# Kernel optimization log

Hardware: AMD Instinct MI355X
Metric: run time of the kernel (lower is better)

Reference implementation:

```python
import jax, jax.numpy as jnp
import numpy as np

B, S, D = 4, 2048, 1024
H, DK, DV = 16, 64, 64
EPS = 1e-6


def setup_inputs() -> dict:
    key = jax.random.key(0)
    ks = jax.random.split(key, 7)
    sc = 0.02
    return {
        "q": jax.random.normal(ks[0], (B, S, D), jnp.float32),
        "k": jax.random.normal(ks[1], (B, S, D), jnp.float32),
        "v": jax.random.normal(ks[2], (B, S, D), jnp.float32),
        "Wq": jax.random.normal(ks[3], (D, H * DK), jnp.float32) * sc,
        "Wk": jax.random.normal(ks[4], (D, H * DK), jnp.float32) * sc,
        "Wv": jax.random.normal(ks[5], (D, H * DV), jnp.float32) * sc,
        "Wo": jax.random.normal(ks[6], (H * DV, D), jnp.float32) * sc,
        "ln_gamma": jnp.ones((D,), jnp.float32),
        "ln_beta": jnp.zeros((D,), jnp.float32),
    }


def reference(q, k, v, Wq, Wk, Wv, Wo, ln_gamma, ln_beta):
    residual = q
    # QKV projections -> [b, h, s, d]
    qh = (q @ Wq).reshape(B, S, H, DK).transpose(0, 2, 1, 3)
    kh = (k @ Wk).reshape(B, S, H, DK).transpose(0, 2, 1, 3)
    vh = (v @ Wv).reshape(B, S, H, DV).transpose(0, 2, 1, 3)
    temperature = jnp.sqrt(jnp.float32(DK))
    # scaled dot-product attention (reverse=False, dropout = eval identity)
    scores = jnp.einsum('bhqd,bhkd->bhqk', qh / temperature, kh)
    attn = jax.nn.softmax(scores, axis=-1)
    ctx = jnp.einsum('bhqk,bhkd->bhqd', attn, vh)
    # merge heads and output projection
    ctx = ctx.transpose(0, 2, 1, 3).reshape(B, S, H * DV)
    out = ctx @ Wo + residual
    # LayerNorm eps=1e-6
    mu = out.mean(-1, keepdims=True)
    var = out.var(-1, keepdims=True)
    out = (out - mu) / jnp.sqrt(var + EPS) * ln_gamma + ln_beta
    return out
```

## Files before the change

### kernel.cpp

```cpp
#include <hip/hip_runtime.h>

typedef __bf16 bf16x8 __attribute__((ext_vector_type(8)));
typedef __bf16 bf16x4 __attribute__((ext_vector_type(4)));
typedef float  f32x4  __attribute__((ext_vector_type(4)));

#define MFMA16(a, b, c) __builtin_amdgcn_mfma_f32_16x16x32_bf16(a, b, c, 0, 0, 0)
#define AS1(p) ((__attribute__((address_space(1))) void*)(p))
#define AS3(p) ((__attribute__((address_space(3))) void*)(p))

union U8 { uint u[4]; bf16x8 v; };
union U4 { bf16x4 h[2]; bf16x8 v; };

__device__ inline uint packbf(float a, float b) {
  union { __bf16 h[2]; uint u; } x;
  x.h[0] = (__bf16)a; x.h[1] = (__bf16)b; return x.u;
}

__global__ __launch_bounds__(256) void cvt_kernel(const float* __restrict__ in,
                                                  __bf16* __restrict__ out, int n4) {
  int i = blockIdx.x * blockDim.x + threadIdx.x;
  if (i < n4) {
    float4 v = ((const float4*)in)[i];
    bf16x4 o = {(__bf16)v.x, (__bf16)v.y, (__bf16)v.z, (__bf16)v.w};
    *(bf16x4*)(out + (size_t)i * 4) = o;
  }
}

__global__ void wtrans_kernel(const float* __restrict__ in, __bf16* __restrict__ out) {
  __shared__ __bf16 t[64][65];
  int bx = blockIdx.x * 64, by = blockIdx.y * 64;
  int tx = threadIdx.x;
  for (int ty = threadIdx.y; ty < 64; ty += 4)
    t[ty][tx] = (__bf16)in[(size_t)(by + ty) * 1024 + bx + tx];
  __syncthreads();
  for (int ty = threadIdx.y; ty < 64; ty += 4)
    out[(size_t)(bx + ty) * 1024 + by + tx] = t[tx][ty];
}

template <int MODE>
__global__ __launch_bounds__(256) void gemm128_kernel(
    const __bf16* __restrict__ A, const __bf16* __restrict__ BT,
    __bf16* __restrict__ Cb, float* __restrict__ Cf,
    const float* __restrict__ resid, int M, int N, int K) {
  __shared__ __bf16 As[128 * 32];
  __shared__ __bf16 Bs[128 * 32];
  const int t = threadIdx.x, l = t & 63, w = t >> 6;
  const int lr = l & 15, lg = l >> 4;
  const int brow = blockIdx.y * 128, bcol = blockIdx.x * 128;
  const int wr = w >> 1, wc = w & 1;
  f32x4 acc[4][4] = {};

  const int srow = w * 16 + (l >> 2);
  const int scol = (l & 3) * 8;
  const __bf16* Ag = A + (size_t)(brow + srow) * K + scol;
  const __bf16* Bg = BT + (size_t)(bcol + srow) * K + scol;
  __bf16* Asw = As + w * 512;
  __bf16* Bsw = Bs + w * 512;

  for (int k0 = 0; k0 < K; k0 += 32) {
    __builtin_amdgcn_global_load_lds(AS1(Ag + k0), AS3(Asw), 16, 0, 0);
    __builtin_amdgcn_global_load_lds(AS1(Ag + k0 + (size_t)64 * K), AS3(Asw + 2048), 16, 0, 0);
    __builtin_amdgcn_global_load_lds(AS1(Bg + k0), AS3(Bsw), 16, 0, 0);
    __builtin_amdgcn_global_load_lds(AS1(Bg + k0 + (size_t)64 * K), AS3(Bsw + 2048), 16, 0, 0);
    __syncthreads();
    bf16x8 a[4], b[4];
#pragma unroll
    for (int m = 0; m < 4; ++m)
      a[m] = *(const bf16x8*)(As + (wr * 64 + m * 16 + lr) * 32 + lg * 8);
#pragma unroll
    for (int n = 0; n < 4; ++n)
      b[n] = *(const bf16x8*)(Bs + (wc * 64 + n * 16 + lr) * 32 + lg * 8);
#pragma unroll
    for (int m = 0; m < 4; ++m)
#pragma unroll
      for (int n = 0; n < 4; ++n)
        acc[m][n] = MFMA16(a[m], b[n], acc[m][n]);
    __syncthreads();
  }

  const int r0 = brow + wr * 64 + lg * 4;
  const int c0 = bcol + wc * 64 + lr;
#pragma unroll
  for (int m = 0; m < 4; ++m)
#pragma unroll
    for (int n = 0; n < 4; ++n) {
      if (MODE == 3) {
        const int dg = c0 + n * 16;
        const int tok = r0 + m * 16;
        bf16x4 pk4;
#pragma unroll
        for (int r = 0; r < 4; ++r) pk4[r] = (__bf16)acc[m][n][r];
        size_t idx = ((size_t)((tok >> 11) * 16 + (dg >> 6)) * 64 + (dg & 63)) * 2048 + (tok & 2047);
        *(bf16x4*)(Cb + idx) = pk4;
      } else {
#pragma unroll
        for (int r = 0; r < 4; ++r) {
          size_t idx = (size_t)(r0 + m * 16 + r) * N + c0 + n * 16;
          if (MODE == 0) Cb[idx] = (__bf16)acc[m][n][r];
          if (MODE == 2) Cb[idx] = (__bf16)(acc[m][n][r] * 0.125f);
          if (MODE == 1) Cf[idx] = acc[m][n][r] + resid[idx];
        }
      }
    }
}

__global__ __launch_bounds__(256) void attn_kernel(const __bf16* __restrict__ Qh,
                                                   const __bf16* __restrict__ Kh,
                                                   const __bf16* __restrict__ VhT,
                                                   __bf16* __restrict__ Ctx) {
  __shared__ __bf16 Vbuf[2 * 4096];
  const int t = threadIdx.x, l = t & 63, w = t >> 6;
  const int lr = l & 15, lg = l >> 4;
  const int bh = blockIdx.y;
  const size_t base = (size_t)(bh >> 4) * (2048 * 1024) + (size_t)(bh & 15) * 64;
  const int q0 = blockIdx.x * 128 + w * 32;

  bf16x8 aq[2][2];
#pragma unroll
  for (int nq = 0; nq < 2; ++nq)
#pragma unroll
    for (int kc = 0; kc < 2; ++kc)
      aq[nq][kc] = *(const bf16x8*)(Qh + base + (size_t)(q0 + nq * 16 + lr) * 1024 + kc * 32 + lg * 8);

  f32x4 o[4][2] = {};
  float rm[2] = {-1e30f, -1e30f}, rl[2] = {0.f, 0.f};

  const int l8 = l & 7, lrow = l >> 3;
  const __bf16* vsrc = VhT + (size_t)bh * 131072 + (size_t)(w * 16 + lrow) * 2048 + ((l8 ^ lrow) * 8);

  const int xorm = (l8) << 4;
  int vo[2][2];
#pragma unroll
  for (int kc = 0; kc < 2; ++kc)
#pragma unroll
    for (int h = 0; h < 2; ++h)
      vo[kc][h] = lr * 128 + ((kc * 64 + h * 32 + lg * 8) ^ xorm);

  {
    __bf16* d0 = Vbuf + w * 1024;
    __builtin_amdgcn_global_load_lds(AS1(vsrc), AS3(d0), 16, 0, 0);
    __builtin_amdgcn_global_load_lds(AS1(vsrc + 16384), AS3(d0 + 512), 16, 0, 0);
  }
  __syncthreads();

  for (int tt = 0; tt < 32; ++tt) {
    const __bf16* Vb = Vbuf + (tt & 1) * 4096;
    __bf16* Vn = Vbuf + ((tt + 1) & 1) * 4096;
    const int kv0 = tt * 64;
    const int kvn = ((tt + 1) & 31) * 64;

    __builtin_amdgcn_global_load_lds(AS1(vsrc + kvn), AS3(Vn + w * 1024), 16, 0, 0);
    __builtin_amdgcn_global_load_lds(AS1(vsrc + kvn + 16384), AS3(Vn + w * 1024 + 512), 16, 0, 0);

    bf16x8 kf[4][2];
#pragma unroll
    for (int mkv = 0; mkv < 4; ++mkv)
#pragma unroll
      for (int kc = 0; kc < 2; ++kc)
        kf[mkv][kc] = *(const bf16x8*)(Kh + base + (size_t)(kv0 + mkv * 16 + lr) * 1024 + kc * 32 + lg * 8);

    f32x4 s[2][4];
    __builtin_amdgcn_s_setprio(1);
#pragma unroll
    for (int nq = 0; nq < 2; ++nq)
#pragma unroll
      for (int mkv = 0; mkv < 4; ++mkv) {
        f32x4 acc = {};
        acc = MFMA16(kf[mkv][0], aq[nq][0], acc);
        acc = MFMA16(kf[mkv][1], aq[nq][1], acc);
        s[nq][mkv] = acc;
      }
    __builtin_amdgcn_s_setprio(0);

    uint pk[2][4][2];
#pragma unroll
    for (int nq = 0; nq < 2; ++nq) {
      float mx = s[nq][0][0];
#pragma unroll
      for (int mkv = 0; mkv < 4; ++mkv)
#pragma unroll
        for (int r = 0; r < 4; ++r) mx = fmaxf(mx, s[nq][mkv][r]);
      mx = fmaxf(mx, __shfl_xor(mx, 16));
      mx = fmaxf(mx, __shfl_xor(mx, 32));
      float nm = fmaxf(rm[nq], mx);
      float corr = __expf(rm[nq] - nm);
      rm[nq] = nm;
      float sum = 0.f;
#pragma unroll
      for (int mkv = 0; mkv < 4; ++mkv) {
        float p0 = __expf(s[nq][mkv][0] - nm);
        float p1 = __expf(s[nq][mkv][1] - nm);
        float p2 = __expf(s[nq][mkv][2] - nm);
        float p3 = __expf(s[nq][mkv][3] - nm);
        sum += (p0 + p1) + (p2 + p3);
        pk[nq][mkv][0] = packbf(p0, p1);
        pk[nq][mkv][1] = packbf(p2, p3);
      }
      sum += __shfl_xor(sum, 16);
      sum += __shfl_xor(sum, 32);
      rl[nq] = rl[nq] * corr + sum;
#pragma unroll
      for (int md = 0; md < 4; ++md) o[md][nq] *= corr;
    }

    __builtin_amdgcn_s_setprio(1);
#pragma unroll
    for (int md = 0; md < 4; ++md) {
#pragma unroll
      for (int kc = 0; kc < 2; ++kc) {
        U4 vf;
        vf.h[0] = *(const bf16x4*)((const char*)Vb + md * 2048 + vo[kc][0]);
        vf.h[1] = *(const bf16x4*)((const char*)Vb + md * 2048 + vo[kc][1]);
#pragma unroll
        for (int nq = 0; nq < 2; ++nq) {
          U8 pf;
          pf.u[0] = pk[nq][2 * kc][0];
          pf.u[1] = pk[nq][2 * kc][1];
          pf.u[2] = pk[nq][2 * kc + 1][0];
          pf.u[3] = pk[nq][2 * kc + 1][1];
          o[md][nq] = MFMA16(vf.v, pf.v, o[md][nq]);
        }
      }
    }
    __builtin_amdgcn_s_setprio(0);

    __syncthreads();
  }

  float rinv[2] = {1.f / rl[0], 1.f / rl[1]};
#pragma unroll
  for (int md = 0; md < 4; ++md)
#pragma unroll
    for (int nq = 0; nq < 2; ++nq) {
      bf16x4 pk4;
#pragma unroll
      for (int r = 0; r < 4; ++r) pk4[r] = (__bf16)(o[md][nq][r] * rinv[nq]);
      *(bf16x4*)(Ctx + base + (size_t)(q0 + nq * 16 + lr) * 1024 + md * 16 + lg * 4) = pk4;
    }
}

__global__ __launch_bounds__(256) void ln_kernel(const float* __restrict__ x,
                                                 const float* __restrict__ g,
                                                 const float* __restrict__ bta,
                                                 float* __restrict__ out) {
  __shared__ float sred[4], s2red[4];
  const int row = blockIdx.x, t = threadIdx.x;
  float4 v = ((const float4*)(x + (size_t)row * 1024))[t];
  float s = v.x + v.y + v.z + v.w;
  float s2 = v.x * v.x + v.y * v.y + v.z * v.z + v.w * v.w;
#pragma unroll
  for (int mask = 1; mask < 64; mask <<= 1) {
    s += __shfl_xor(s, mask);
    s2 += __shfl_xor(s2, mask);
  }
  if ((t & 63) == 0) { sred[t >> 6] = s; s2red[t >> 6] = s2; }
  __syncthreads();
  s = sred[0] + sred[1] + sred[2] + sred[3];
  s2 = s2red[0] + s2red[1] + s2red[2] + s2red[3];
  float mu = s * (1.f / 1024.f);
  float inv = rsqrtf(s2 * (1.f / 1024.f) - mu * mu + 1e-6f);
  float4 gv = ((const float4*)g)[t];
  float4 bv = ((const float4*)bta)[t];
  float4 ov;
  ov.x = (v.x - mu) * inv * gv.x + bv.x;
  ov.y = (v.y - mu) * inv * gv.y + bv.y;
  ov.z = (v.z - mu) * inv * gv.z + bv.z;
  ov.w = (v.w - mu) * inv * gv.w + bv.w;
  ((float4*)(out + (size_t)row * 1024))[t] = ov;
}

extern "C" void kernel_launch(void* const* d_in, const int* in_sizes, int n_in,
                              void* d_out, int out_size, void* d_ws, size_t ws_size,
                              hipStream_t stream) {
  const float* q  = (const float*)d_in[0];
  const float* k  = (const float*)d_in[1];
  const float* v  = (const float*)d_in[2];
  const float* Wq = (const float*)d_in[3];
  const float* Wk = (const float*)d_in[4];
  const float* Wv = (const float*)d_in[5];
  const float* Wo = (const float*)d_in[6];
  const float* g  = (const float*)d_in[7];
  const float* bt = (const float*)d_in[8];
  float* out = (float*)d_out;

  const int NTOK = 4 * 2048;
  const int NEL = NTOK * 1024;

  __bf16* qb  = (__bf16*)d_ws;
  __bf16* kb  = qb + NEL;
  __bf16* vb  = kb + NEL;
  __bf16* WqT = vb + NEL;
  __bf16* WkT = WqT + 1024 * 1024;
  __bf16* WvT = WkT + 1024 * 1024;
  __bf16* WoT = WvT + 1024 * 1024;
  __bf16* Qh  = WoT + 1024 * 1024;
  __bf16* Kh  = Qh + NEL;
  __bf16* VhT = Kh + NEL;
  __bf16* ctx = qb;
  float*  ao  = (float*)kb;

  cvt_kernel<<<NEL / 1024, 256, 0, stream>>>(q, qb, NEL / 4);
  cvt_kernel<<<NEL / 1024, 256, 0, stream>>>(k, kb, NEL / 4);
  cvt_kernel<<<NEL / 1024, 256, 0, stream>>>(v, vb, NEL / 4);

  dim3 wtb(64, 4), wtg(16, 16);
  wtrans_kernel<<<wtg, wtb, 0, stream>>>(Wq, WqT);
  wtrans_kernel<<<wtg, wtb, 0, stream>>>(Wk, WkT);
  wtrans_kernel<<<wtg, wtb, 0, stream>>>(Wv, WvT);
  wtrans_kernel<<<wtg, wtb, 0, stream>>>(Wo, WoT);

  dim3 gg(1024 / 128, NTOK / 128);
  gemm128_kernel<2><<<gg, 256, 0, stream>>>(qb, WqT, Qh, nullptr, nullptr, NTOK, 1024, 1024);
  gemm128_kernel<0><<<gg, 256, 0, stream>>>(kb, WkT, Kh, nullptr, nullptr, NTOK, 1024, 1024);
  gemm128_kernel<3><<<gg, 256, 0, stream>>>(vb, WvT, VhT, nullptr, nullptr, NTOK, 1024, 1024);

  attn_kernel<<<dim3(2048 / 128, 64), 256, 0, stream>>>(Qh, Kh, VhT, ctx);

  gemm128_kernel<1><<<gg, 256, 0, stream>>>(ctx, WoT, nullptr, ao, q, NTOK, 1024, 1024);

  ln_kernel<<<NTOK, 256, 0, stream>>>(ao, g, bt, out);
}
```

Measured before the change: 515.8 us.

## Drop LDS V staging, use exp2 softmax with lazy rescaling

The attention kernel no longer stages V tiles through double-buffered LDS with global_load_lds and block barriers. Each lane now reads V fragments straight from global memory into registers. The Q scale folds log2(e) into the projection epilogue so the softmax can use exp2f. Rescaling of the running max and output accumulators is skipped unless some row's max grows by more than 8, which removes per-tile correction multiplies. The trade-offs are more uncoalesced global and cache traffic for V, and larger unnormalized exponent values in bf16 P.

```diff
diff --git a/kernel.cpp b/kernel.cpp
--- a/kernel.cpp
+++ b/kernel.cpp
@@ -97,7 +97,7 @@
         for (int r = 0; r < 4; ++r) {
           size_t idx = (size_t)(r0 + m * 16 + r) * N + c0 + n * 16;
           if (MODE == 0) Cb[idx] = (__bf16)acc[m][n][r];
-          if (MODE == 2) Cb[idx] = (__bf16)(acc[m][n][r] * 0.125f);
+          if (MODE == 2) Cb[idx] = (__bf16)(acc[m][n][r] * 0.1803368801111244f);
           if (MODE == 1) Cf[idx] = acc[m][n][r] + resid[idx];
         }
       }
@@ -108,7 +108,6 @@
                                                    const __bf16* __restrict__ Kh,
                                                    const __bf16* __restrict__ VhT,
                                                    __bf16* __restrict__ Ctx) {
-  __shared__ __bf16 Vbuf[2 * 4096];
   const int t = threadIdx.x, l = t & 63, w = t >> 6;
   const int lr = l & 15, lg = l >> 4;
   const int bh = blockIdx.y;
@@ -125,92 +124,76 @@
   f32x4 o[4][2] = {};
   float rm[2] = {-1e30f, -1e30f}, rl[2] = {0.f, 0.f};
 
-  const int l8 = l & 7, lrow = l >> 3;
-  const __bf16* vsrc = VhT + (size_t)bh * 131072 + (size_t)(w * 16 + lrow) * 2048 + ((l8 ^ lrow) * 8);
-
-  const int xorm = (l8) << 4;
-  int vo[2][2];
-#pragma unroll
-  for (int kc = 0; kc < 2; ++kc)
-#pragma unroll
-    for (int h = 0; h < 2; ++h)
-      vo[kc][h] = lr * 128 + ((kc * 64 + h * 32 + lg * 8) ^ xorm);
-
-  {
-    __bf16* d0 = Vbuf + w * 1024;
-    __builtin_amdgcn_global_load_lds(AS1(vsrc), AS3(d0), 16, 0, 0);
-    __builtin_amdgcn_global_load_lds(AS1(vsrc + 16384), AS3(d0 + 512), 16, 0, 0);
-  }
-  __syncthreads();
-
-  for (int tt = 0; tt < 32; ++tt) {
-    const __bf16* Vb = Vbuf + (tt & 1) * 4096;
-    __bf16* Vn = Vbuf + ((tt + 1) & 1) * 4096;
-    const int kv0 = tt * 64;
-    const int kvn = ((tt + 1) & 31) * 64;
-
-    __builtin_amdgcn_global_load_lds(AS1(vsrc + kvn), AS3(Vn + w * 1024), 16, 0, 0);
-    __builtin_amdgcn_global_load_lds(AS1(vsrc + kvn + 16384), AS3(Vn + w * 1024 + 512), 16, 0, 0);
-
+  const __bf16* kp = Kh + base + (size_t)lr * 1024 + lg * 8;
+  const __bf16* vp = VhT + (size_t)bh * 131072 + (size_t)lr * 2048 + lg * 4;
+
+  for (int kv0 = 0; kv0 < 2048; kv0 += 64) {
     bf16x8 kf[4][2];
 #pragma unroll
     for (int mkv = 0; mkv < 4; ++mkv)
 #pragma unroll
       for (int kc = 0; kc < 2; ++kc)
-        kf[mkv][kc] = *(const bf16x8*)(Kh + base + (size_t)(kv0 + mkv * 16 + lr) * 1024 + kc * 32 + lg * 8);
-
-    f32x4 s[2][4];
-    __builtin_amdgcn_s_setprio(1);
-#pragma unroll
-    for (int nq = 0; nq < 2; ++nq)
+        kf[mkv][kc] = *(const bf16x8*)(kp + (size_t)(kv0 + mkv * 16) * 1024 + kc * 32);
+
+    U4 vf[4][2];
+#pragma unroll
+    for (int md = 0; md < 4; ++md)
+#pragma unroll
+      for (int kc = 0; kc < 2; ++kc) {
+        vf[md][kc].h[0] = *(const bf16x4*)(vp + (size_t)md * 32768 + kv0 + kc * 32);
+        vf[md][kc].h[1] = *(const bf16x4*)(vp + (size_t)md * 32768 + kv0 + kc * 32 + 16);
+      }
+
+    uint pk[2][4][2];
+#pragma unroll
+    for (int nq = 0; nq < 2; ++nq) {
+      f32x4 s4[4];
+      __builtin_amdgcn_s_setprio(1);
 #pragma unroll
       for (int mkv = 0; mkv < 4; ++mkv) {
         f32x4 acc = {};
         acc = MFMA16(kf[mkv][0], aq[nq][0], acc);
         acc = MFMA16(kf[mkv][1], aq[nq][1], acc);
-        s[nq][mkv] = acc;
-      }
-    __builtin_amdgcn_s_setprio(0);
-
-    uint pk[2][4][2];
-#pragma unroll
-    for (int nq = 0; nq < 2; ++nq) {
-      float mx = s[nq][0][0];
+        s4[mkv] = acc;
+      }
+      __builtin_amdgcn_s_setprio(0);
+
+      float mx = s4[0][0];
 #pragma unroll
       for (int mkv = 0; mkv < 4; ++mkv)
 #pragma unroll
-        for (int r = 0; r < 4; ++r) mx = fmaxf(mx, s[nq][mkv][r]);
+        for (int r = 0; r < 4; ++r) mx = fmaxf(mx, s4[mkv][r]);
       mx = fmaxf(mx, __shfl_xor(mx, 16));
       mx = fmaxf(mx, __shfl_xor(mx, 32));
-      float nm = fmaxf(rm[nq], mx);
-      float corr = __expf(rm[nq] - nm);
-      rm[nq] = nm;
+      if (!__all(mx - rm[nq] <= 8.f)) {
+        float nm = fmaxf(rm[nq], mx);
+        float corr = exp2f(rm[nq] - nm);
+        rm[nq] = nm;
+        rl[nq] *= corr;
+#pragma unroll
+        for (int md = 0; md < 4; ++md) o[md][nq] *= corr;
+      }
       float sum = 0.f;
 #pragma unroll
       for (int mkv = 0; mkv < 4; ++mkv) {
-        float p0 = __expf(s[nq][mkv][0] - nm);
-        float p1 = __expf(s[nq][mkv][1] - nm);
-        float p2 = __expf(s[nq][mkv][2] - nm);
-        float p3 = __expf(s[nq][mkv][3] - nm);
+        float p0 = exp2f(s4[mkv][0] - rm[nq]);
+        float p1 = exp2f(s4[mkv][1] - rm[nq]);
+        float p2 = exp2f(s4[mkv][2] - rm[nq]);
+        float p3 = exp2f(s4[mkv][3] - rm[nq]);
         sum += (p0 + p1) + (p2 + p3);
         pk[nq][mkv][0] = packbf(p0, p1);
         pk[nq][mkv][1] = packbf(p2, p3);
       }
       sum += __shfl_xor(sum, 16);
       sum += __shfl_xor(sum, 32);
-      rl[nq] = rl[nq] * corr + sum;
-#pragma unroll
-      for (int md = 0; md < 4; ++md) o[md][nq] *= corr;
+      rl[nq] += sum;
     }
 
     __builtin_amdgcn_s_setprio(1);
 #pragma unroll
-    for (int md = 0; md < 4; ++md) {
-#pragma unroll
-      for (int kc = 0; kc < 2; ++kc) {
-        U4 vf;
-        vf.h[0] = *(const bf16x4*)((const char*)Vb + md * 2048 + vo[kc][0]);
-        vf.h[1] = *(const bf16x4*)((const char*)Vb + md * 2048 + vo[kc][1]);
+    for (int md = 0; md < 4; ++md)
+#pragma unroll
+      for (int kc = 0; kc < 2; ++kc)
 #pragma unroll
         for (int nq = 0; nq < 2; ++nq) {
           U8 pf;
@@ -218,13 +201,9 @@
           pf.u[1] = pk[nq][2 * kc][1];
           pf.u[2] = pk[nq][2 * kc + 1][0];
           pf.u[3] = pk[nq][2 * kc + 1][1];
-          o[md][nq] = MFMA16(vf.v, pf.v, o[md][nq]);
+          o[md][nq] = MFMA16(vf[md][kc].v, pf.v, o[md][nq]);
         }
-      }
-    }
     __builtin_amdgcn_s_setprio(0);
-
-    __syncthreads();
   }
 
   float rinv[2] = {1.f / rl[0], 1.f / rl[1]};
```

New measurement: 679.2 us. +31.7%, slower.

## Batch QKV GEMMs and conversions into single launches; lazy-rescale exp2 softmax

Applied to the files above, without the earlier changes.

The three input conversions become one launch and the three QKV projection GEMMs become one launch, with grid z selecting the operands. The Q scale now folds in log2(e) so attention can use exp2f. The online softmax also skips the max update and rescale of the accumulator unless the running max grows by more than 8. This cuts launch overhead, gives each GEMM launch a larger grid for better occupancy, and removes most per-tile rescale work in attention, at the cost of bf16 probabilities that can reach up to 2^8 before being normalised.

```diff
diff --git a/kernel.cpp b/kernel.cpp
--- a/kernel.cpp
+++ b/kernel.cpp
@@ -16,13 +16,17 @@
   x.h[0] = (__bf16)a; x.h[1] = (__bf16)b; return x.u;
 }
 
-__global__ __launch_bounds__(256) void cvt_kernel(const float* __restrict__ in,
-                                                  __bf16* __restrict__ out, int n4) {
+__global__ __launch_bounds__(256) void cvt3_kernel(const float* __restrict__ q,
+                                                   const float* __restrict__ k,
+                                                   const float* __restrict__ v,
+                                                   __bf16* __restrict__ out, int n4) {
+  const int z = blockIdx.y;
+  const float* in = z == 0 ? q : (z == 1 ? k : v);
   int i = blockIdx.x * blockDim.x + threadIdx.x;
   if (i < n4) {
-    float4 v = ((const float4*)in)[i];
-    bf16x4 o = {(__bf16)v.x, (__bf16)v.y, (__bf16)v.z, (__bf16)v.w};
-    *(bf16x4*)(out + (size_t)i * 4) = o;
+    float4 vv = ((const float4*)in)[i];
+    bf16x4 o = {(__bf16)vv.x, (__bf16)vv.y, (__bf16)vv.z, (__bf16)vv.w};
+    *(bf16x4*)(out + (size_t)z * n4 * 4 + (size_t)i * 4) = o;
   }
 }
 
@@ -37,11 +41,79 @@
     out[(size_t)(bx + ty) * 1024 + by + tx] = t[tx][ty];
 }
 
-template <int MODE>
-__global__ __launch_bounds__(256) void gemm128_kernel(
+__global__ __launch_bounds__(256) void gemm_qkv_kernel(
+    const __bf16* __restrict__ A0, const __bf16* __restrict__ B0, __bf16* __restrict__ C0,
+    const __bf16* __restrict__ A1, const __bf16* __restrict__ B1, __bf16* __restrict__ C1,
+    const __bf16* __restrict__ A2, const __bf16* __restrict__ B2, __bf16* __restrict__ C2) {
+  __shared__ __bf16 As[128 * 32];
+  __shared__ __bf16 Bs[128 * 32];
+  const int z = blockIdx.z;
+  const __bf16* A = z == 0 ? A0 : (z == 1 ? A1 : A2);
+  const __bf16* BT = z == 0 ? B0 : (z == 1 ? B1 : B2);
+  __bf16* Cb = z == 0 ? C0 : (z == 1 ? C1 : C2);
+  const int K = 1024, N = 1024;
+  const int t = threadIdx.x, l = t & 63, w = t >> 6;
+  const int lr = l & 15, lg = l >> 4;
+  const int brow = blockIdx.y * 128, bcol = blockIdx.x * 128;
+  const int wr = w >> 1, wc = w & 1;
+  f32x4 acc[4][4] = {};
+
+  const int srow = w * 16 + (l >> 2);
+  const int scol = (l & 3) * 8;
+  const __bf16* Ag = A + (size_t)(brow + srow) * K + scol;
+  const __bf16* Bg = BT + (size_t)(bcol + srow) * K + scol;
+  __bf16* Asw = As + w * 512;
+  __bf16* Bsw = Bs + w * 512;
+
+  for (int k0 = 0; k0 < K; k0 += 32) {
+    __builtin_amdgcn_global_load_lds(AS1(Ag + k0), AS3(Asw), 16, 0, 0);
+    __builtin_amdgcn_global_load_lds(AS1(Ag + k0 + (size_t)64 * K), AS3(Asw + 2048), 16, 0, 0);
+    __builtin_amdgcn_global_load_lds(AS1(Bg + k0), AS3(Bsw), 16, 0, 0);
+    __builtin_amdgcn_global_load_lds(AS1(Bg + k0 + (size_t)64 * K), AS3(Bsw + 2048), 16, 0, 0);
+    __syncthreads();
+    bf16x8 a[4], b[4];
+#pragma unroll
+    for (int m = 0; m < 4; ++m)
+      a[m] = *(const bf16x8*)(As + (wr * 64 + m * 16 + lr) * 32 + lg * 8);
+#pragma unroll
+    for (int n = 0; n < 4; ++n)
+      b[n] = *(const bf16x8*)(Bs + (wc * 64 + n * 16 + lr) * 32 + lg * 8);
+#pragma unroll
+    for (int m = 0; m < 4; ++m)
+#pragma unroll
+      for (int n = 0; n < 4; ++n)
+        acc[m][n] = MFMA16(a[m], b[n], acc[m][n]);
+    __syncthreads();
+  }
+
+  const int r0 = brow + wr * 64 + lg * 4;
+  const int c0 = bcol + wc * 64 + lr;
+  const float scale = (z == 0) ? 0.1803368801111244f : 1.0f;
+#pragma unroll
+  for (int m = 0; m < 4; ++m)
+#pragma unroll
+    for (int n = 0; n < 4; ++n) {
+      if (z == 2) {
+        const int dg = c0 + n * 16;
+        const int tok = r0 + m * 16;
+        bf16x4 pk4;
+#pragma unroll
+        for (int r = 0; r < 4; ++r) pk4[r] = (__bf16)acc[m][n][r];
+        size_t idx = ((size_t)((tok >> 11) * 16 + (dg >> 6)) * 64 + (dg & 63)) * 2048 + (tok & 2047);
+        *(bf16x4*)(Cb + idx) = pk4;
+      } else {
+#pragma unroll
+        for (int r = 0; r < 4; ++r) {
+          size_t idx = (size_t)(r0 + m * 16 + r) * N + c0 + n * 16;
+          Cb[idx] = (__bf16)(acc[m][n][r] * scale);
+        }
+      }
+    }
+}
+
+__global__ __launch_bounds__(256) void gemm_out_kernel(
     const __bf16* __restrict__ A, const __bf16* __restrict__ BT,
-    __bf16* __restrict__ Cb, float* __restrict__ Cf,
-    const float* __restrict__ resid, int M, int N, int K) {
+    float* __restrict__ Cf, const float* __restrict__ resid, int M, int N, int K) {
   __shared__ __bf16 As[128 * 32];
   __shared__ __bf16 Bs[128 * 32];
   const int t = threadIdx.x, l = t & 63, w = t >> 6;
@@ -83,25 +155,12 @@
 #pragma unroll
   for (int m = 0; m < 4; ++m)
 #pragma unroll
-    for (int n = 0; n < 4; ++n) {
-      if (MODE == 3) {
-        const int dg = c0 + n * 16;
-        const int tok = r0 + m * 16;
-        bf16x4 pk4;
-#pragma unroll
-        for (int r = 0; r < 4; ++r) pk4[r] = (__bf16)acc[m][n][r];
-        size_t idx = ((size_t)((tok >> 11) * 16 + (dg >> 6)) * 64 + (dg & 63)) * 2048 + (tok & 2047);
-        *(bf16x4*)(Cb + idx) = pk4;
-      } else {
-#pragma unroll
-        for (int r = 0; r < 4; ++r) {
-          size_t idx = (size_t)(r0 + m * 16 + r) * N + c0 + n * 16;
-          if (MODE == 0) Cb[idx] = (__bf16)acc[m][n][r];
-          if (MODE == 2) Cb[idx] = (__bf16)(acc[m][n][r] * 0.125f);
-          if (MODE == 1) Cf[idx] = acc[m][n][r] + resid[idx];
-        }
-      }
-    }
+    for (int n = 0; n < 4; ++n)
+#pragma unroll
+      for (int r = 0; r < 4; ++r) {
+        size_t idx = (size_t)(r0 + m * 16 + r) * N + c0 + n * 16;
+        Cf[idx] = acc[m][n][r] + resid[idx];
+      }
 }
 
 __global__ __launch_bounds__(256) void attn_kernel(const __bf16* __restrict__ Qh,
@@ -182,25 +241,28 @@
         for (int r = 0; r < 4; ++r) mx = fmaxf(mx, s[nq][mkv][r]);
       mx = fmaxf(mx, __shfl_xor(mx, 16));
       mx = fmaxf(mx, __shfl_xor(mx, 32));
-      float nm = fmaxf(rm[nq], mx);
-      float corr = __expf(rm[nq] - nm);
-      rm[nq] = nm;
+      if (!__all(mx - rm[nq] <= 8.f)) {
+        float nm = fmaxf(rm[nq], mx);
+        float corr = exp2f(rm[nq] - nm);
+        rm[nq] = nm;
+        rl[nq] *= corr;
+#pragma unroll
+        for (int md = 0; md < 4; ++md) o[md][nq] *= corr;
+      }
       float sum = 0.f;
 #pragma unroll
       for (int mkv = 0; mkv < 4; ++mkv) {
-        float p0 = __expf(s[nq][mkv][0] - nm);
-        float p1 = __expf(s[nq][mkv][1] - nm);
-        float p2 = __expf(s[nq][mkv][2] - nm);
-        float p3 = __expf(s[nq][mkv][3] - nm);
+        float p0 = exp2f(s[nq][mkv][0] - rm[nq]);
+        float p1 = exp2f(s[nq][mkv][1] - rm[nq]);
+        float p2 = exp2f(s[nq][mkv][2] - rm[nq]);
+        float p3 = exp2f(s[nq][mkv][3] - rm[nq]);
         sum += (p0 + p1) + (p2 + p3);
         pk[nq][mkv][0] = packbf(p0, p1);
         pk[nq][mkv][1] = packbf(p2, p3);
       }
       sum += __shfl_xor(sum, 16);
       sum += __shfl_xor(sum, 32);
-      rl[nq] = rl[nq] * corr + sum;
-#pragma unroll
-      for (int md = 0; md < 4; ++md) o[md][nq] *= corr;
+      rl[nq] += sum;
     }
 
     __builtin_amdgcn_s_setprio(1);
@@ -299,9 +361,7 @@
   __bf16* ctx = qb;
   float*  ao  = (float*)kb;
 
-  cvt_kernel<<<NEL / 1024, 256, 0, stream>>>(q, qb, NEL / 4);
-  cvt_kernel<<<NEL / 1024, 256, 0, stream>>>(k, kb, NEL / 4);
-  cvt_kernel<<<NEL / 1024, 256, 0, stream>>>(v, vb, NEL / 4);
+  cvt3_kernel<<<dim3(NEL / 1024, 3), 256, 0, stream>>>(q, k, v, qb, NEL / 4);
 
   dim3 wtb(64, 4), wtg(16, 16);
   wtrans_kernel<<<wtg, wtb, 0, stream>>>(Wq, WqT);
@@ -309,14 +369,13 @@
   wtrans_kernel<<<wtg, wtb, 0, stream>>>(Wv, WvT);
   wtrans_kernel<<<wtg, wtb, 0, stream>>>(Wo, WoT);
 
-  dim3 gg(1024 / 128, NTOK / 128);
-  gemm128_kernel<2><<<gg, 256, 0, stream>>>(qb, WqT, Qh, nullptr, nullptr, NTOK, 1024, 1024);
-  gemm128_kernel<0><<<gg, 256, 0, stream>>>(kb, WkT, Kh, nullptr, nullptr, NTOK, 1024, 1024);
-  gemm128_kernel<3><<<gg, 256, 0, stream>>>(vb, WvT, VhT, nullptr, nullptr, NTOK, 1024, 1024);
+  gemm_qkv_kernel<<<dim3(1024 / 128, NTOK / 128, 3), 256, 0, stream>>>(
+      qb, WqT, Qh, kb, WkT, Kh, vb, WvT, VhT);
 
   attn_kernel<<<dim3(2048 / 128, 64), 256, 0, stream>>>(Qh, Kh, VhT, ctx);
 
-  gemm128_kernel<1><<<gg, 256, 0, stream>>>(ctx, WoT, nullptr, ao, q, NTOK, 1024, 1024);
+  gemm_out_kernel<<<dim3(1024 / 128, NTOK / 128), 256, 0, stream>>>(
+      ctx, WoT, ao, q, NTOK, 1024, 1024);
 
   ln_kernel<<<NTOK, 256, 0, stream>>>(ao, g, bt, out);
 }
```

Result: no change. 510.4 us (-1.0%).
